# Kernel optimization log

Hardware: AMD Instinct MI355X
Metric: run time of the kernel (lower is better)

The kernel has to match this reference:

```python
import jax, jax.numpy as jnp
import numpy as np

B, N, C, H = 16, 1024, 768, 12
D = C // H
SCALE = D ** -0.5


def setup_inputs() -> dict:
    key = jax.random.key(0)
    k1, k2, k3, k4, k5 = jax.random.split(key, 5)
    return {
        "x": jax.random.normal(k1, (B, N, C), dtype=jnp.float32),
        "qkv_w": jax.random.normal(k2, (3 * C, C), dtype=jnp.float32) * (C ** -0.5),
        "qkv_b": jax.random.normal(k3, (3 * C,), dtype=jnp.float32) * 0.02,
        "proj_w": jax.random.normal(k4, (C, C), dtype=jnp.float32) * (C ** -0.5),
        "proj_b": jax.random.normal(k5, (C,), dtype=jnp.float32) * 0.02,
    }


def reference(x, qkv_w, qkv_b, proj_w, proj_b):
    # x: [B, N, C]. torch Linear: y = x @ W.T + b
    b, n, c = x.shape
    qkv = x @ qkv_w.T + qkv_b                      # [B, N, 3C]
    qkv = qkv.reshape(b, n, 3, H, D).transpose(2, 0, 3, 1, 4)  # [3, B, H, N, D]
    q, k, v = qkv[0], qkv[1], qkv[2]
    # dropout is identity in eval mode; scores scaled by head_dim**-0.5
    scores = jnp.einsum("bhnd,bhmd->bhnm", q, k) * SCALE  # [B, H, N, N]
    attn = jax.nn.softmax(scores, axis=-1)
    out = jnp.einsum("bhnm,bhmd->bhnd", attn, v)           # [B, H, N, D]
    out = out.transpose(0, 2, 1, 3).reshape(b, n, c)       # [B, N, C]
    return out @ proj_w.T + proj_b
```

## Files before the change

kernel.cpp:

```cpp
#include <hip/hip_runtime.h>
#include <hip/hip_bf16.h>


typedef __attribute__((ext_vector_type(8))) short short8;
typedef __attribute__((ext_vector_type(4))) float floatx4;
typedef __attribute__((ext_vector_type(16))) float floatx16;

constexpr int Bsz = 16, Nseq = 1024, Cdim = 768, Hh = 12, Dd = 64;
constexpr float SCALE = 0.125f;
constexpr float QSC = 0.1803368801f;

__device__ __forceinline__ ushort f2bs(float f) {
    union { __hip_bfloat16 h; ushort u; } cv;
    cv.h = __float2bfloat16(f);
    return cv.u;
}
__device__ __forceinline__ void stF(float* p, float v) { *p = v; }
__device__ __forceinline__ void stF(ushort* p, float v) { *p = f2bs(v); }

__device__ __forceinline__ void gld16(void* lds, const void* g) {
    __builtin_amdgcn_global_load_lds(
        (const __attribute__((address_space(1))) unsigned int*)g,
        (__attribute__((address_space(3))) unsigned int*)lds, 16, 0, 0);
}

__global__ __launch_bounds__(256) void pack_bf16(
        const float* __restrict__ x, const float* __restrict__ w1,
        const float* __restrict__ w2, ushort* __restrict__ xb,
        ushort* __restrict__ w1b, ushort* __restrict__ w2b) {
    const size_t n0 = (size_t)Bsz * Nseq * Cdim;
    const size_t n1 = (size_t)3 * Cdim * Cdim;
    size_t i = ((size_t)blockIdx.x * 256 + threadIdx.x) * 4;
    const float* src;
    ushort* dst;
    if (i < n0) { src = x; dst = xb; }
    else if (i < n0 + n1) { i -= n0; src = w1; dst = w1b; }
    else { i -= n0 + n1; src = w2; dst = w2b; }
    float4 v = *(const float4*)&src[i];
    *(ushort4*)&dst[i] = make_ushort4(f2bs(v.x), f2bs(v.y), f2bs(v.z), f2bs(v.w));
}

template <typename TO>
__global__ __launch_bounds__(256) void gemm_nt_mfma(
        const ushort* __restrict__ A, const ushort* __restrict__ Bw,
        const float* __restrict__ bias, TO* __restrict__ C0,
        ushort* __restrict__ vt, int split, int ld0,
        int M, int N, int K, int vmode, int qsplit, float qscale) {
    __shared__ ushort As[128 * 64];
    __shared__ ushort Bs[128 * 64];
    const int t = threadIdx.x;
    const int lane = t & 63;
    const int w = t >> 6;
    const int quad = lane >> 4;
    const int l16 = lane & 15;
    const int m0 = blockIdx.y * 128;
    const int n0 = blockIdx.x * 128;
    const int mw = (w >> 1) * 64;
    const int nw = (w & 1) * 64;
    const int srow = lane >> 3;
    const int schunk = lane & 7;

    floatx4 acc[4][4];
#pragma unroll
    for (int i = 0; i < 4; ++i)
#pragma unroll
        for (int j = 0; j < 4; ++j) acc[i][j] = (floatx4)0.0f;

    for (int k0 = 0; k0 < K; k0 += 64) {
        __syncthreads();
#pragma unroll
        for (int i = 0; i < 4; ++i) {
            int r0 = (w * 4 + i) * 8;
            int row = r0 + srow;
            int cs = (schunk ^ (row & 7)) * 8;
            gld16(&As[r0 * 64], &A[(size_t)(m0 + row) * K + k0 + cs]);
            gld16(&Bs[r0 * 64], &Bw[(size_t)(n0 + row) * K + k0 + cs]);
        }
        __syncthreads();

#pragma unroll
        for (int kk = 0; kk < 2; ++kk) {
            const int pc = ((kk * 4 + quad) ^ (l16 & 7)) * 8;
            short8 af[4], bfr[4];
#pragma unroll
            for (int i = 0; i < 4; ++i)
                af[i] = *(const short8*)&As[(mw + i * 16 + l16) * 64 + pc];
#pragma unroll
            for (int j = 0; j < 4; ++j)
                bfr[j] = *(const short8*)&Bs[(nw + j * 16 + l16) * 64 + pc];
#pragma unroll
            for (int i = 0; i < 4; ++i)
#pragma unroll
                for (int j = 0; j < 4; ++j)
                    acc[i][j] = __builtin_amdgcn_mfma_f32_16x16x32_bf16(
                        af[i], bfr[j], acc[i][j], 0, 0, 0);
        }
    }

#pragma unroll
    for (int j = 0; j < 4; ++j) {
        int col = n0 + nw + j * 16 + l16;
        float bc = bias[col];
        float sc = (col < qsplit) ? qscale : 1.0f;
        if (vmode && col >= split) {
            int ch = col - split;
            int h = ch >> 6, d = ch & 63;
#pragma unroll
            for (int i = 0; i < 4; ++i)
#pragma unroll
                for (int r = 0; r < 4; ++r) {
                    int row = m0 + mw + i * 16 + quad * 4 + r;
                    int b = row >> 10, n = row & 1023;
                    vt[(((size_t)(b * Hh + h)) * Dd + d) * Nseq + n] =
                        f2bs(acc[i][j][r] + bc);
                }
        } else {
#pragma unroll
            for (int i = 0; i < 4; ++i)
#pragma unroll
                for (int r = 0; r < 4; ++r) {
                    int row = m0 + mw + i * 16 + quad * 4 + r;
                    stF(&C0[(size_t)row * ld0 + col], (acc[i][j][r] + bc) * sc);
                }
        }
    }
}

__global__ __launch_bounds__(256, 3) void attn_mfma(
        const ushort* __restrict__ qk, const ushort* __restrict__ vt,
        ushort* __restrict__ outp) {
    __shared__ ushort Ks[2][64 * 64];
    __shared__ ushort Vts[2][64 * 64];

    const int t = threadIdx.x;
    const int lane = t & 63;
    const int w = t >> 6;
    const int l32 = lane & 31;
    const int hi = lane >> 5;
    const int srow = lane >> 3;
    const int schunk = lane & 7;

    const int bid = blockIdx.x;
    const int qt = (bid >> 3) & 7;
    const int bh = (bid & 7) + 8 * (bid >> 6);
    const int h = bh % Hh, b = bh / Hh;

    const size_t rs = 2 * Cdim;
    const ushort* qbase = qk + (size_t)b * Nseq * rs + h * Dd;
    const ushort* kbase = qbase + Cdim;
    const ushort* vbase = vt + (size_t)bh * Dd * Nseq;

    short8 aq[4];
    {
        int q = qt * 128 + w * 32 + l32;
#pragma unroll
        for (int kc = 0; kc < 4; ++kc)
            aq[kc] = *(const short8*)&qbase[(size_t)q * rs + kc * 16 + hi * 8];
    }

    auto stage = [&](int kt64, int buf) {
#pragma unroll
        for (int i = 0; i < 2; ++i) {
            int r0 = (w * 2 + i) * 8;
            int row = r0 + srow;
            int cs = (schunk ^ (row & 7)) * 8;
            gld16(&Ks[buf][r0 * 64], &kbase[(size_t)(kt64 * 64 + row) * rs + cs]);
            gld16(&Vts[buf][r0 * 64], &vbase[(size_t)row * Nseq + kt64 * 64 + cs]);
        }
    };

    floatx16 o[2];
    o[0] = (floatx16)0.0f;
    o[1] = (floatx16)0.0f;
    float lsum = 0.f;

    stage(0, 0);
    for (int kt = 0; kt < Nseq / 64; ++kt) {
        __syncthreads();
        if (kt + 1 < Nseq / 64) stage(kt + 1, (kt + 1) & 1);
        const ushort* Kb = Ks[kt & 1];
        const ushort* Vb = Vts[kt & 1];

        floatx16 st[2];
        st[0] = (floatx16)0.0f;
        st[1] = (floatx16)0.0f;
#pragma unroll
        for (int kc = 0; kc < 4; ++kc) {
            const int cs = ((kc * 2 + hi) ^ (l32 & 7)) * 8;
            short8 ak0 = *(const short8*)&Kb[l32 * 64 + cs];
            short8 ak1 = *(const short8*)&Kb[(32 + l32) * 64 + cs];
            st[0] = __builtin_amdgcn_mfma_f32_32x32x16_bf16(ak0, aq[kc], st[0], 0, 0, 0);
            st[1] = __builtin_amdgcn_mfma_f32_32x32x16_bf16(ak1, aq[kc], st[1], 0, 0, 0);
        }

#pragma unroll
        for (int km = 0; km < 2; ++km) {
            float p[16];
#pragma unroll
            for (int r = 0; r < 16; ++r) p[r] = exp2f(st[km][r]);
            lsum += (((p[0] + p[1]) + (p[2] + p[3])) +
                     ((p[4] + p[5]) + (p[6] + p[7]))) +
                    (((p[8] + p[9]) + (p[10] + p[11])) +
                     ((p[12] + p[13]) + (p[14] + p[15])));
            uint c[8];
#pragma unroll
            for (int i = 0; i < 8; ++i)
                c[i] = (uint)f2bs(p[2 * i]) | ((uint)f2bs(p[2 * i + 1]) << 16);
            uint x0 = __shfl_xor(c[0], 32), x1 = __shfl_xor(c[1], 32);
            uint x2 = __shfl_xor(c[2], 32), x3 = __shfl_xor(c[3], 32);
            union { uint u[4]; short8 s; } af0, af1;
            af0.u[0] = hi ? x2 : c[0];
            af0.u[1] = hi ? x3 : c[1];
            af0.u[2] = hi ? c[2] : x0;
            af0.u[3] = hi ? c[3] : x1;
            uint x4 = __shfl_xor(c[4], 32), x5 = __shfl_xor(c[5], 32);
            uint x6 = __shfl_xor(c[6], 32), x7 = __shfl_xor(c[7], 32);
            af1.u[0] = hi ? x6 : c[4];
            af1.u[1] = hi ? x7 : c[5];
            af1.u[2] = hi ? c[6] : x4;
            af1.u[3] = hi ? c[7] : x5;

#pragma unroll
            for (int dblk = 0; dblk < 2; ++dblk) {
                const int row = dblk * 32 + l32;
#pragma unroll
                for (int ks = 0; ks < 2; ++ks) {
                    const int ch = ((km * 4 + ks * 2 + hi) ^ (l32 & 7)) * 8;
                    short8 bv = *(const short8*)&Vb[row * 64 + ch];
                    o[dblk] = __builtin_amdgcn_mfma_f32_32x32x16_bf16(
                        ks ? af1.s : af0.s, bv, o[dblk], 0, 0, 0);
                }
            }
        }
    }

    float lf = lsum + __shfl_xor(lsum, 32);
    float linv = __builtin_amdgcn_rcpf(lf);

    const int qg0 = qt * 128 + w * 32;
#pragma unroll
    for (int r = 0; r < 16; ++r) {
        int rowq = (r & 3) + 8 * (r >> 2) + 4 * hi;
        float li = __shfl(linv, rowq);
        int q = qg0 + rowq;
#pragma unroll
        for (int dblk = 0; dblk < 2; ++dblk) {
            int d = dblk * 32 + l32;
            outp[((size_t)(b * Nseq + q)) * Cdim + h * Dd + d] =
                f2bs(o[dblk][r] * li);
        }
    }
}

extern "C" void kernel_launch(void* const* d_in, const int* in_sizes, int n_in,
                              void* d_out, int out_size, void* d_ws, size_t ws_size,
                              hipStream_t stream) {
    const float* x      = (const float*)d_in[0];
    const float* qkv_w  = (const float*)d_in[1];
    const float* qkv_b  = (const float*)d_in[2];
    const float* proj_w = (const float*)d_in[3];
    const float* proj_b = (const float*)d_in[4];
    float* out = (float*)d_out;

    const int M = Bsz * Nseq;
    ushort* xb    = (ushort*)d_ws;
    ushort* qk    = xb + (size_t)M * Cdim;
    ushort* vtbuf = qk + (size_t)M * 2 * Cdim;
    ushort* wqkvb = vtbuf + (size_t)Hh * Bsz * Dd * Nseq;
    ushort* wprjb = wqkvb + (size_t)3 * Cdim * Cdim;
    ushort* attnout = xb;

    pack_bf16<<<14592, 256, 0, stream>>>(x, qkv_w, proj_w, xb, wqkvb, wprjb);
    gemm_nt_mfma<ushort><<<dim3(18, 128), 256, 0, stream>>>(
        xb, wqkvb, qkv_b, qk, vtbuf, 2 * Cdim, 2 * Cdim, M, 3 * Cdim, Cdim, 1,
        Cdim, QSC);
    attn_mfma<<<Bsz * Hh * (Nseq / 128), 256, 0, stream>>>(qk, vtbuf, attnout);
    gemm_nt_mfma<float><<<dim3(6, 128), 256, 0, stream>>>(
        attnout, wprjb, proj_b, out, vtbuf, 1 << 30, Cdim, M, Cdim, Cdim, 0,
        0, 1.0f);
}
```

Before: 316.1 us.

## Compute V transposed via swapped-operand GEMM and use permlane32 swap in attention

The V projection moves out of the QKV GEMM into a separate GEMM with swapped operands (W_v times x), so V^T is written directly as [C, B*N] with coalesced stores and a row-wise bias, instead of the old scattered per-element transposed stores. Attention now reads V^T with the new stride. The softmax inner loop uses the native exp2 builtin, packed float2-to-bf16 conversion and permlane32_swap in place of shfl_xor plus selects. This costs an extra kernel launch and makes the V GEMM reread x, in exchange for removing uncoalesced writes and cutting cross-lane traffic in attention.

```diff
diff --git a/kernel.cpp b/kernel.cpp
--- a/kernel.cpp
+++ b/kernel.cpp
@@ -5,10 +5,11 @@
 typedef __attribute__((ext_vector_type(8))) short short8;
 typedef __attribute__((ext_vector_type(4))) float floatx4;
 typedef __attribute__((ext_vector_type(16))) float floatx16;
+typedef __attribute__((ext_vector_type(2))) unsigned int uint2v;
 
 constexpr int Bsz = 16, Nseq = 1024, Cdim = 768, Hh = 12, Dd = 64;
-constexpr float SCALE = 0.125f;
 constexpr float QSC = 0.1803368801f;
+constexpr int LDV = Bsz * Nseq;
 
 __device__ __forceinline__ ushort f2bs(float f) {
     union { __hip_bfloat16 h; ushort u; } cv;
@@ -17,6 +18,14 @@
 }
 __device__ __forceinline__ void stF(float* p, float v) { *p = v; }
 __device__ __forceinline__ void stF(ushort* p, float v) { *p = f2bs(v); }
+
+__device__ __forceinline__ float fexp2(float x) {
+#if __has_builtin(__builtin_amdgcn_exp2f)
+    return __builtin_amdgcn_exp2f(x);
+#else
+    return exp2f(x);
+#endif
+}
 
 __device__ __forceinline__ void gld16(void* lds, const void* g) {
     __builtin_amdgcn_global_load_lds(
@@ -44,8 +53,7 @@
 __global__ __launch_bounds__(256) void gemm_nt_mfma(
         const ushort* __restrict__ A, const ushort* __restrict__ Bw,
         const float* __restrict__ bias, TO* __restrict__ C0,
-        ushort* __restrict__ vt, int split, int ld0,
-        int M, int N, int K, int vmode, int qsplit, float qscale) {
+        int ld0, int M, int N, int K, int bias_row, int qsplit, float qscale) {
     __shared__ ushort As[128 * 64];
     __shared__ ushort Bs[128 * 64];
     const int t = threadIdx.x;
@@ -97,24 +105,30 @@
         }
     }
 
-#pragma unroll
-    for (int j = 0; j < 4; ++j) {
-        int col = n0 + nw + j * 16 + l16;
-        float bc = bias[col];
-        float sc = (col < qsplit) ? qscale : 1.0f;
-        if (vmode && col >= split) {
-            int ch = col - split;
-            int h = ch >> 6, d = ch & 63;
+    if (bias_row) {
+        float brv[4][4];
+#pragma unroll
+        for (int i = 0; i < 4; ++i)
+#pragma unroll
+            for (int r = 0; r < 4; ++r)
+                brv[i][r] = bias[m0 + mw + i * 16 + quad * 4 + r];
+#pragma unroll
+        for (int j = 0; j < 4; ++j) {
+            int col = n0 + nw + j * 16 + l16;
 #pragma unroll
             for (int i = 0; i < 4; ++i)
 #pragma unroll
                 for (int r = 0; r < 4; ++r) {
                     int row = m0 + mw + i * 16 + quad * 4 + r;
-                    int b = row >> 10, n = row & 1023;
-                    vt[(((size_t)(b * Hh + h)) * Dd + d) * Nseq + n] =
-                        f2bs(acc[i][j][r] + bc);
+                    stF(&C0[(size_t)row * ld0 + col], acc[i][j][r] + brv[i][r]);
                 }
-        } else {
+        }
+    } else {
+#pragma unroll
+        for (int j = 0; j < 4; ++j) {
+            int col = n0 + nw + j * 16 + l16;
+            float bc = bias[col];
+            float sc = (col < qsplit) ? qscale : 1.0f;
 #pragma unroll
             for (int i = 0; i < 4; ++i)
 #pragma unroll
@@ -148,7 +162,7 @@
     const size_t rs = 2 * Cdim;
     const ushort* qbase = qk + (size_t)b * Nseq * rs + h * Dd;
     const ushort* kbase = qbase + Cdim;
-    const ushort* vbase = vt + (size_t)bh * Dd * Nseq;
+    const ushort* vbase = vt + (size_t)(h * Dd) * LDV + (size_t)b * Nseq;
 
     short8 aq[4];
     {
@@ -165,7 +179,7 @@
             int row = r0 + srow;
             int cs = (schunk ^ (row & 7)) * 8;
             gld16(&Ks[buf][r0 * 64], &kbase[(size_t)(kt64 * 64 + row) * rs + cs]);
-            gld16(&Vts[buf][r0 * 64], &vbase[(size_t)row * Nseq + kt64 * 64 + cs]);
+            gld16(&Vts[buf][r0 * 64], &vbase[(size_t)row * LDV + kt64 * 64 + cs]);
         }
     };
 
@@ -197,28 +211,41 @@
         for (int km = 0; km < 2; ++km) {
             float p[16];
 #pragma unroll
-            for (int r = 0; r < 16; ++r) p[r] = exp2f(st[km][r]);
+            for (int r = 0; r < 16; ++r) p[r] = fexp2(st[km][r]);
             lsum += (((p[0] + p[1]) + (p[2] + p[3])) +
                      ((p[4] + p[5]) + (p[6] + p[7]))) +
                     (((p[8] + p[9]) + (p[10] + p[11])) +
                      ((p[12] + p[13]) + (p[14] + p[15])));
             uint c[8];
 #pragma unroll
-            for (int i = 0; i < 8; ++i)
-                c[i] = (uint)f2bs(p[2 * i]) | ((uint)f2bs(p[2 * i + 1]) << 16);
+            for (int i = 0; i < 8; ++i) {
+                union { __hip_bfloat162 h2; uint u; } cv;
+                cv.h2 = __float22bfloat162_rn(make_float2(p[2 * i], p[2 * i + 1]));
+                c[i] = cv.u;
+            }
+            uint wd[8];
+#if __has_builtin(__builtin_amdgcn_permlane32_swap)
+            uint2v r02 = __builtin_amdgcn_permlane32_swap(c[0], c[2], false, false);
+            uint2v r13 = __builtin_amdgcn_permlane32_swap(c[1], c[3], false, false);
+            uint2v r46 = __builtin_amdgcn_permlane32_swap(c[4], c[6], false, false);
+            uint2v r57 = __builtin_amdgcn_permlane32_swap(c[5], c[7], false, false);
+            wd[0] = r02.x; wd[2] = r02.y;
+            wd[1] = r13.x; wd[3] = r13.y;
+            wd[4] = r46.x; wd[6] = r46.y;
+            wd[5] = r57.x; wd[7] = r57.y;
+#else
             uint x0 = __shfl_xor(c[0], 32), x1 = __shfl_xor(c[1], 32);
             uint x2 = __shfl_xor(c[2], 32), x3 = __shfl_xor(c[3], 32);
-            union { uint u[4]; short8 s; } af0, af1;
-            af0.u[0] = hi ? x2 : c[0];
-            af0.u[1] = hi ? x3 : c[1];
-            af0.u[2] = hi ? c[2] : x0;
-            af0.u[3] = hi ? c[3] : x1;
             uint x4 = __shfl_xor(c[4], 32), x5 = __shfl_xor(c[5], 32);
             uint x6 = __shfl_xor(c[6], 32), x7 = __shfl_xor(c[7], 32);
-            af1.u[0] = hi ? x6 : c[4];
-            af1.u[1] = hi ? x7 : c[5];
-            af1.u[2] = hi ? c[6] : x4;
-            af1.u[3] = hi ? c[7] : x5;
+            wd[0] = hi ? x2 : c[0]; wd[1] = hi ? x3 : c[1];
+            wd[2] = hi ? c[2] : x0; wd[3] = hi ? c[3] : x1;
+            wd[4] = hi ? x6 : c[4]; wd[5] = hi ? x7 : c[5];
+            wd[6] = hi ? c[6] : x4; wd[7] = hi ? c[7] : x5;
+#endif
+            union { uint u[4]; short8 s; } af0, af1;
+            af0.u[0] = wd[0]; af0.u[1] = wd[1]; af0.u[2] = wd[2]; af0.u[3] = wd[3];
+            af1.u[0] = wd[4]; af1.u[1] = wd[5]; af1.u[2] = wd[6]; af1.u[3] = wd[7];
 
 #pragma unroll
             for (int dblk = 0; dblk < 2; ++dblk) {
@@ -266,16 +293,17 @@
     ushort* xb    = (ushort*)d_ws;
     ushort* qk    = xb + (size_t)M * Cdim;
     ushort* vtbuf = qk + (size_t)M * 2 * Cdim;
-    ushort* wqkvb = vtbuf + (size_t)Hh * Bsz * Dd * Nseq;
+    ushort* wqkvb = vtbuf + (size_t)Cdim * M;
     ushort* wprjb = wqkvb + (size_t)3 * Cdim * Cdim;
     ushort* attnout = xb;
 
     pack_bf16<<<14592, 256, 0, stream>>>(x, qkv_w, proj_w, xb, wqkvb, wprjb);
-    gemm_nt_mfma<ushort><<<dim3(18, 128), 256, 0, stream>>>(
-        xb, wqkvb, qkv_b, qk, vtbuf, 2 * Cdim, 2 * Cdim, M, 3 * Cdim, Cdim, 1,
-        Cdim, QSC);
+    gemm_nt_mfma<ushort><<<dim3(12, 128), 256, 0, stream>>>(
+        xb, wqkvb, qkv_b, qk, 2 * Cdim, M, 2 * Cdim, Cdim, 0, Cdim, QSC);
+    gemm_nt_mfma<ushort><<<dim3(128, 6), 256, 0, stream>>>(
+        wqkvb + (size_t)2 * Cdim * Cdim, xb, qkv_b + 2 * Cdim, vtbuf,
+        M, Cdim, M, Cdim, 1, 0, 1.0f);
     attn_mfma<<<Bsz * Hh * (Nseq / 128), 256, 0, stream>>>(qk, vtbuf, attnout);
     gemm_nt_mfma<float><<<dim3(6, 128), 256, 0, stream>>>(
-        attnout, wprjb, proj_b, out, vtbuf, 1 << 30, Cdim, M, Cdim, Cdim, 0,
-        0, 1.0f);
-}
+        attnout, wprjb, proj_b, out, Cdim, M, Cdim, Cdim, 0, 0, 1.0f);
+}
```

Result: faster. 299.3 us (-5.3%).
